# Optimization experiments

Measured on AMD Instinct MI355X. Metric: run time of the kernel, lower is better.

The kernel has to match this reference:

```python
import jax, jax.numpy as jnp
import numpy as np

N, C, H, W = 16, 128, 128, 128


def setup_inputs() -> dict:
    key = jax.random.key(0)
    ks = jax.random.split(key, 7)
    s = 0.02
    return {
        "x": jax.random.normal(ks[0], (N, C, H, W), dtype=jnp.float32),
        "w_key": jax.random.normal(ks[1], (C, C), dtype=jnp.float32) * s,
        "b_key": jax.random.normal(ks[2], (C,), dtype=jnp.float32) * s,
        "w_query": jax.random.normal(ks[3], (C, C), dtype=jnp.float32) * s,
        "b_query": jax.random.normal(ks[4], (C,), dtype=jnp.float32) * s,
        "w_value": jax.random.normal(ks[5], (C, C), dtype=jnp.float32) * s,
        "b_value": jax.random.normal(ks[6], (C,), dtype=jnp.float32) * s,
        "gamma": jnp.zeros((1,), dtype=jnp.float32),
    }


def _conv1x1(x, w, b):
    # 1x1 conv: (N,C,H,W) x (O,C) -> (N,O,H,W)
    return jnp.einsum('nchw,oc->nohw', x, w) + b[None, :, None, None]


def reference(x, w_key, b_key, w_query, b_query, w_value, b_value, gamma):
    k = _conv1x1(x, w_key, b_key)
    q = _conv1x1(x, w_query, b_query)
    v = _conv1x1(x, w_value, b_value)
    k_size = x.shape[1]  # output_channel
    scale = jnp.asarray(k_size, x.dtype) ** 0.5
    # similarity[n,o,w,v] = sum_h k[n,o,h,w] * q[n,o,h,v]  (k^T over H @ q)
    sim = jnp.einsum('nohw,nohv->nowv', k, q) / scale
    # softmax over dim=2 (the first W axis)
    attn = jax.nn.softmax(sim, axis=2)
    # out[n,o,h,v] = sum_w v[n,o,h,w] * attn[n,o,w,v]
    out = jnp.einsum('nohw,nowv->nohv', v, attn)
    return gamma[0] * out + x
```

## Files before the change

### kernel.cpp

```cpp
#include <hip/hip_runtime.h>
#include <hip/hip_bf16.h>
#include <math.h>

#define CN      128
#define HWN     16384
#define NBATCH  16
#define PLANE   (CN * HWN)
#define TSTRIDE ((size_t)NBATCH * PLANE)

typedef __attribute__((ext_vector_type(8))) short  short8;
typedef __attribute__((ext_vector_type(4))) float  float4v;

__device__ __forceinline__ unsigned short f2b(float f) {
    __hip_bfloat16 h = __float2bfloat16(f);
    return *reinterpret_cast<unsigned short*>(&h);
}
__device__ __forceinline__ unsigned packbf(float lo, float hi) {
    return (unsigned)f2b(lo) | ((unsigned)f2b(hi) << 16);
}
__device__ __forceinline__ float bf2f(unsigned short u) {
    union { unsigned i; float f; } x; x.i = ((unsigned)u) << 16; return x.f;
}

__global__ void prep_kernel(const float* __restrict__ wk, const float* __restrict__ bk,
                            const float* __restrict__ wq, const float* __restrict__ bq,
                            const float* __restrict__ wv, const float* __restrict__ bv,
                            unsigned short* __restrict__ wbf, float* __restrict__ bias)
{
    int i = blockIdx.x * 256 + threadIdx.x;
    int tensor = i >> 14, oc = i & 16383;
    const float* w = tensor == 0 ? wk : (tensor == 1 ? wq : wv);
    wbf[i] = f2b(w[oc]);
    if (i < 384) {
        const float* b = i < 128 ? bk : (i < 256 ? bq : bv);
        bias[i] = b[i & 127];
    }
}

__global__ __launch_bounds__(256) void kqv_kernel(
    const float* __restrict__ x, const unsigned short* __restrict__ wbf,
    const float* __restrict__ bias, unsigned short* __restrict__ kqv)
{
    __shared__ unsigned Xl[64 * 68];

    const int n   = blockIdx.y;
    const int hw0 = blockIdx.x * 64;
    const int t    = threadIdx.x;
    const int lane = t & 63, wv = t >> 6;
    const int l15  = lane & 15, quad = lane >> 4;

    const float* xp = x + (size_t)n * PLANE + hw0 + lane;
    #pragma unroll
    for (int it = 0; it < 4; ++it) {
        const int c0 = (wv * 4 + it) * 8;
        float v[8];
        #pragma unroll
        for (int j = 0; j < 8; ++j) v[j] = xp[(size_t)(c0 + j) * HWN];
        uint4 u;
        u.x = packbf(v[0], v[1]); u.y = packbf(v[2], v[3]);
        u.z = packbf(v[4], v[5]); u.w = packbf(v[6], v[7]);
        *(uint4*)&Xl[lane * 68 + c0 / 2] = u;
    }
    __syncthreads();

    short8 bfr[4][4];
    #pragma unroll
    for (int nt = 0; nt < 4; ++nt)
        #pragma unroll
        for (int k = 0; k < 4; ++k)
            bfr[nt][k] = *(const short8*)&Xl[(nt * 16 + l15) * 68 + quad * 4 + k * 16];

    for (int mt = 0; mt < 6; ++mt) {
        const int o0 = wv * 96 + mt * 16;
        short8 afr[4];
        #pragma unroll
        for (int k = 0; k < 4; ++k)
            afr[k] = *(const short8*)&wbf[(o0 + l15) * CN + quad * 8 + k * 32];
        float b0 = bias[o0 + quad * 4 + 0], b1 = bias[o0 + quad * 4 + 1];
        float b2 = bias[o0 + quad * 4 + 2], b3 = bias[o0 + quad * 4 + 3];

        #pragma unroll
        for (int nt = 0; nt < 4; ++nt) {
            float4v acc = {b0, b1, b2, b3};
            #pragma unroll
            for (int k = 0; k < 4; ++k)
                acc = __builtin_amdgcn_mfma_f32_16x16x32_bf16(afr[k], bfr[nt][k], acc, 0, 0, 0);
            #pragma unroll
            for (int r = 0; r < 4; ++r) {
                const int oo = o0 + quad * 4 + r;
                const size_t idx = (size_t)(oo >> 7) * TSTRIDE
                                 + ((size_t)n * CN + (oo & 127)) * HWN
                                 + hw0 + nt * 16 + l15;
                kqv[idx] = f2b(acc[r]);
            }
        }
    }
}

__global__ __launch_bounds__(256) void attn_kernel(
    const unsigned short* __restrict__ kqv, const float* __restrict__ x,
    const float* __restrict__ gamma, float* __restrict__ out)
{
    __shared__ unsigned lds[17408];
    unsigned* Kt = lds;
    unsigned* Qt = lds + 8704;
    unsigned short* At = (unsigned short*)lds;

    const int no = blockIdx.x;
    const unsigned short* Kg = kqv + (size_t)no * HWN;
    const unsigned short* Qg = Kg + TSTRIDE;
    const unsigned short* Vg = Kg + 2 * TSTRIDE;

    const int t = threadIdx.x, lane = t & 63, wv = t >> 6;
    const int l15 = lane & 15, quad = lane >> 4;

    #pragma unroll
    for (int p = 0; p < 8; ++p) {
        const int w  = (p & 1) * 64 + lane;
        const int h0 = ((p >> 1) * 4 + wv) * 8;
        unsigned short kv[8], qv[8];
        #pragma unroll
        for (int j = 0; j < 8; ++j) {
            kv[j] = Kg[(h0 + j) * 128 + w];
            qv[j] = Qg[(h0 + j) * 128 + w];
        }
        uint4 a, b;
        a.x = (unsigned)kv[0] | ((unsigned)kv[1] << 16); a.y = (unsigned)kv[2] | ((unsigned)kv[3] << 16);
        a.z = (unsigned)kv[4] | ((unsigned)kv[5] << 16); a.w = (unsigned)kv[6] | ((unsigned)kv[7] << 16);
        b.x = (unsigned)qv[0] | ((unsigned)qv[1] << 16); b.y = (unsigned)qv[2] | ((unsigned)qv[3] << 16);
        b.z = (unsigned)qv[4] | ((unsigned)qv[5] << 16); b.w = (unsigned)qv[6] | ((unsigned)qv[7] << 16);
        *(uint4*)&Kt[w * 68 + h0 / 2] = a;
        *(uint4*)&Qt[w * 68 + h0 / 2] = b;
    }
    __syncthreads();

    const int v0 = wv * 32;
    float4v acc1[2][8];
    #pragma unroll
    for (int mt = 0; mt < 2; ++mt)
        #pragma unroll
        for (int nt = 0; nt < 8; ++nt) acc1[mt][nt] = (float4v){0.f, 0.f, 0.f, 0.f};

    {
        short8 afr[2][4];
        #pragma unroll
        for (int mt = 0; mt < 2; ++mt)
            #pragma unroll
            for (int k = 0; k < 4; ++k)
                afr[mt][k] = *(const short8*)&Qt[(v0 + mt * 16 + l15) * 68 + quad * 4 + k * 16];
        #pragma unroll
        for (int nt = 0; nt < 8; ++nt) {
            short8 bfr[4];
            #pragma unroll
            for (int k = 0; k < 4; ++k)
                bfr[k] = *(const short8*)&Kt[(nt * 16 + l15) * 68 + quad * 4 + k * 16];
            #pragma unroll
            for (int mt = 0; mt < 2; ++mt)
                #pragma unroll
                for (int k = 0; k < 4; ++k)
                    acc1[mt][nt] = __builtin_amdgcn_mfma_f32_16x16x32_bf16(afr[mt][k], bfr[k], acc1[mt][nt], 0, 0, 0);
        }
    }
    __syncthreads();

    const float sc = 0.08838834764831845f;
    #pragma unroll
    for (int mt = 0; mt < 2; ++mt)
        #pragma unroll
        for (int r = 0; r < 4; ++r) {
            float m = -INFINITY;
            #pragma unroll
            for (int nt = 0; nt < 8; ++nt) {
                acc1[mt][nt][r] *= sc;
                m = fmaxf(m, acc1[mt][nt][r]);
            }
            #pragma unroll
            for (int d = 1; d < 16; d <<= 1) m = fmaxf(m, __shfl_xor(m, d, 64));
            float s = 0.f;
            #pragma unroll
            for (int nt = 0; nt < 8; ++nt) {
                const float e = __expf(acc1[mt][nt][r] - m);
                acc1[mt][nt][r] = e;
                s += e;
            }
            #pragma unroll
            for (int d = 1; d < 16; d <<= 1) s += __shfl_xor(s, d, 64);
            const float inv = 1.0f / s;
            const int v = v0 + mt * 16 + quad * 4 + r;
            #pragma unroll
            for (int nt = 0; nt < 8; ++nt)
                At[v * 136 + nt * 16 + l15] = f2b(acc1[mt][nt][r] * inv);
        }
    __syncthreads();

    const int h0 = wv * 32;
    float4v acc2[2][8];
    #pragma unroll
    for (int mt = 0; mt < 2; ++mt)
        #pragma unroll
        for (int nt = 0; nt < 8; ++nt) acc2[mt][nt] = (float4v){0.f, 0.f, 0.f, 0.f};

    {
        short8 vfr[2][4];
        #pragma unroll
        for (int mt = 0; mt < 2; ++mt)
            #pragma unroll
            for (int k = 0; k < 4; ++k)
                vfr[mt][k] = *(const short8*)&Vg[(h0 + mt * 16 + l15) * 128 + quad * 8 + k * 32];
        #pragma unroll
        for (int nt = 0; nt < 8; ++nt) {
            short8 bfr[4];
            #pragma unroll
            for (int k = 0; k < 4; ++k)
                bfr[k] = *(const short8*)&At[(nt * 16 + l15) * 136 + quad * 8 + k * 32];
            #pragma unroll
            for (int mt = 0; mt < 2; ++mt)
                #pragma unroll
                for (int k = 0; k < 4; ++k)
                    acc2[mt][nt] = __builtin_amdgcn_mfma_f32_16x16x32_bf16(vfr[mt][k], bfr[k], acc2[mt][nt], 0, 0, 0);
        }
    }

    const float g = gamma[0];
    const float* xp = x + (size_t)no * HWN;
    float*       op = out + (size_t)no * HWN;
    #pragma unroll
    for (int mt = 0; mt < 2; ++mt)
        #pragma unroll
        for (int nt = 0; nt < 8; ++nt)
            #pragma unroll
            for (int r = 0; r < 4; ++r) {
                const int h = h0 + mt * 16 + quad * 4 + r;
                const int v = nt * 16 + l15;
                const int idx = h * 128 + v;
                op[idx] = fmaf(g, acc2[mt][nt][r], xp[idx]);
            }
}

extern "C" void kernel_launch(void* const* d_in, const int* in_sizes, int n_in,
                              void* d_out, int out_size, void* d_ws, size_t ws_size,
                              hipStream_t stream) {
    const float* x     = (const float*)d_in[0];
    const float* wk    = (const float*)d_in[1];
    const float* bk    = (const float*)d_in[2];
    const float* wq    = (const float*)d_in[3];
    const float* bq    = (const float*)d_in[4];
    const float* wv    = (const float*)d_in[5];
    const float* bv    = (const float*)d_in[6];
    const float* gamma = (const float*)d_in[7];
    float* out = (float*)d_out;

    unsigned short* wbf  = (unsigned short*)d_ws;
    float*          bias = (float*)((char*)d_ws + (192 << 10));
    unsigned short* kqv  = (unsigned short*)((char*)d_ws + (256 << 10));

    prep_kernel<<<192, 256, 0, stream>>>(wk, bk, wq, bq, wv, bv, wbf, bias);
    dim3 gA(HWN / 64, NBATCH);
    kqv_kernel<<<gA, 256, 0, stream>>>(x, wbf, bias, kqv);
    attn_kernel<<<NBATCH * CN, 256, 0, stream>>>(kqv, x, gamma, out);
}
```

Measured before the change: 429.1 us.

## Store K and Q in pre-transposed h8-blocked layout so attention skips LDS staging

After: 476.6 us. +11.1%, slower.

```diff
diff --git a/kernel.cpp b/kernel.cpp
--- a/kernel.cpp
+++ b/kernel.cpp
@@ -17,9 +17,6 @@
 }
 __device__ __forceinline__ unsigned packbf(float lo, float hi) {
     return (unsigned)f2b(lo) | ((unsigned)f2b(hi) << 16);
-}
-__device__ __forceinline__ float bf2f(unsigned short u) {
-    union { unsigned i; float f; } x; x.i = ((unsigned)u) << 16; return x.f;
 }
 
 __global__ void prep_kernel(const float* __restrict__ wk, const float* __restrict__ bk,
@@ -41,57 +38,97 @@
     const float* __restrict__ x, const unsigned short* __restrict__ wbf,
     const float* __restrict__ bias, unsigned short* __restrict__ kqv)
 {
-    __shared__ unsigned Xl[64 * 68];
-
-    const int n   = blockIdx.y;
-    const int hw0 = blockIdx.x * 64;
-    const int t    = threadIdx.x;
-    const int lane = t & 63, wv = t >> 6;
-    const int l15  = lane & 15, quad = lane >> 4;
-
-    const float* xp = x + (size_t)n * PLANE + hw0 + lane;
-    #pragma unroll
-    for (int it = 0; it < 4; ++it) {
-        const int c0 = (wv * 4 + it) * 8;
-        float v[8];
-        #pragma unroll
-        for (int j = 0; j < 8; ++j) v[j] = xp[(size_t)(c0 + j) * HWN];
-        uint4 u;
-        u.x = packbf(v[0], v[1]); u.y = packbf(v[2], v[3]);
-        u.z = packbf(v[4], v[5]); u.w = packbf(v[6], v[7]);
-        *(uint4*)&Xl[lane * 68 + c0 / 2] = u;
-    }
-    __syncthreads();
-
-    short8 bfr[4][4];
-    #pragma unroll
-    for (int nt = 0; nt < 4; ++nt)
-        #pragma unroll
-        for (int k = 0; k < 4; ++k)
-            bfr[nt][k] = *(const short8*)&Xl[(nt * 16 + l15) * 68 + quad * 4 + k * 16];
-
-    for (int mt = 0; mt < 6; ++mt) {
-        const int o0 = wv * 96 + mt * 16;
-        short8 afr[4];
-        #pragma unroll
-        for (int k = 0; k < 4; ++k)
-            afr[k] = *(const short8*)&wbf[(o0 + l15) * CN + quad * 8 + k * 32];
-        float b0 = bias[o0 + quad * 4 + 0], b1 = bias[o0 + quad * 4 + 1];
-        float b2 = bias[o0 + quad * 4 + 2], b3 = bias[o0 + quad * 4 + 3];
-
-        #pragma unroll
-        for (int nt = 0; nt < 4; ++nt) {
-            float4v acc = {b0, b1, b2, b3};
-            #pragma unroll
-            for (int k = 0; k < 4; ++k)
-                acc = __builtin_amdgcn_mfma_f32_16x16x32_bf16(afr[k], bfr[nt][k], acc, 0, 0, 0);
-            #pragma unroll
-            for (int r = 0; r < 4; ++r) {
-                const int oo = o0 + quad * 4 + r;
-                const size_t idx = (size_t)(oo >> 7) * TSTRIDE
-                                 + ((size_t)n * CN + (oo & 127)) * HWN
-                                 + hw0 + nt * 16 + l15;
-                kqv[idx] = f2b(acc[r]);
+    __shared__ unsigned Xc[128 * 68];
+    __shared__ unsigned short Tk[4][16 * 136];
+
+    const int h8 = blockIdx.x >> 2, wq = blockIdx.x & 3, n = blockIdx.y;
+    const int h0 = h8 * 8;
+    const int t = threadIdx.x, lane = t & 63, wv = t >> 6;
+    const int l15 = lane & 15, quad = lane >> 4;
+    unsigned short* T = Tk[wv];
+
+    for (int chunk = 0; chunk < 2; ++chunk) {
+        const int w0 = wq * 32 + chunk * 16;
+        __syncthreads();
+
+        {
+            const int hwl = t & 127, half = t >> 7;
+            const int wl = hwl >> 3, dh = hwl & 7;
+            const float* xp = x + (size_t)n * PLANE + (size_t)(h0 + dh) * 128 + w0 + wl;
+            #pragma unroll
+            for (int i = 0; i < 8; ++i) {
+                const int c0 = (half * 8 + i) * 8;
+                float v[8];
+                #pragma unroll
+                for (int cc = 0; cc < 8; ++cc) v[cc] = xp[(size_t)(c0 + cc) * HWN];
+                uint4 u;
+                u.x = packbf(v[0], v[1]); u.y = packbf(v[2], v[3]);
+                u.z = packbf(v[4], v[5]); u.w = packbf(v[6], v[7]);
+                *(uint4*)&Xc[hwl * 68 + c0 / 2] = u;
+            }
+        }
+        __syncthreads();
+
+        short8 afr[8][4];
+        #pragma unroll
+        for (int mt = 0; mt < 8; ++mt)
+            #pragma unroll
+            for (int k = 0; k < 4; ++k)
+                afr[mt][k] = *(const short8*)&Xc[(mt * 16 + l15) * 68 + k * 16 + quad * 4];
+
+        for (int nt = 0; nt < 6; ++nt) {
+            const int ob = (nt * 4 + wv) * 16;
+            short8 bfr[4];
+            #pragma unroll
+            for (int k = 0; k < 4; ++k)
+                bfr[k] = *(const short8*)&wbf[(ob + l15) * CN + k * 32 + quad * 8];
+            const float bb = bias[ob + l15];
+            float4v acc[8];
+            #pragma unroll
+            for (int mt = 0; mt < 8; ++mt) acc[mt] = (float4v){bb, bb, bb, bb};
+            #pragma unroll
+            for (int mt = 0; mt < 8; ++mt)
+                #pragma unroll
+                for (int k = 0; k < 4; ++k)
+                    acc[mt] = __builtin_amdgcn_mfma_f32_16x16x32_bf16(afr[mt][k], bfr[k], acc[mt], 0, 0, 0);
+
+            #pragma unroll
+            for (int mt = 0; mt < 8; ++mt) {
+                uint2 p;
+                p.x = packbf(acc[mt][0], acc[mt][1]);
+                p.y = packbf(acc[mt][2], acc[mt][3]);
+                *(uint2*)&T[l15 * 136 + mt * 16 + quad * 4] = p;
+            }
+
+            const int tensor = ob >> 7;
+            const int oo = ob & 127;
+            if (tensor < 2) {
+                const int row = lane >> 2, s = lane & 3;
+                unsigned short* dst = kqv + (size_t)tensor * TSTRIDE
+                                    + ((size_t)n * CN + oo + row) * HWN + h8 * 1024;
+                #pragma unroll
+                for (int j = 0; j < 4; ++j) {
+                    uint4 u = *(const uint4*)&T[row * 136 + (s + 4 * j) * 8];
+                    *(uint4*)&dst[(w0 + s + 4 * j) * 8] = u;
+                }
+            } else {
+                const int o = lane >> 2, g = lane & 3;
+                const int wlh = g & 1, dh2 = g >> 1;
+                unsigned short* dst = kqv + 2 * TSTRIDE + ((size_t)n * CN + oo + o) * HWN;
+                #pragma unroll
+                for (int j = 0; j < 4; ++j) {
+                    const int dh = j * 2 + dh2;
+                    unsigned short tmp[8];
+                    #pragma unroll
+                    for (int i = 0; i < 8; ++i)
+                        tmp[i] = T[o * 136 + (wlh * 8 + i) * 8 + dh];
+                    uint4 u;
+                    u.x = (unsigned)tmp[0] | ((unsigned)tmp[1] << 16);
+                    u.y = (unsigned)tmp[2] | ((unsigned)tmp[3] << 16);
+                    u.z = (unsigned)tmp[4] | ((unsigned)tmp[5] << 16);
+                    u.w = (unsigned)tmp[6] | ((unsigned)tmp[7] << 16);
+                    *(uint4*)&dst[(size_t)(h0 + dh) * 128 + w0 + wlh * 8] = u;
+                }
             }
         }
     }
@@ -101,67 +138,42 @@
     const unsigned short* __restrict__ kqv, const float* __restrict__ x,
     const float* __restrict__ gamma, float* __restrict__ out)
 {
-    __shared__ unsigned lds[17408];
-    unsigned* Kt = lds;
-    unsigned* Qt = lds + 8704;
-    unsigned short* At = (unsigned short*)lds;
+    __shared__ unsigned short At[128 * 136];
 
     const int no = blockIdx.x;
-    const unsigned short* Kg = kqv + (size_t)no * HWN;
-    const unsigned short* Qg = Kg + TSTRIDE;
-    const unsigned short* Vg = Kg + 2 * TSTRIDE;
+    const unsigned short* KT = kqv + (size_t)no * HWN;
+    const unsigned short* QT = KT + TSTRIDE;
+    const unsigned short* Vg = KT + 2 * TSTRIDE;
 
     const int t = threadIdx.x, lane = t & 63, wv = t >> 6;
     const int l15 = lane & 15, quad = lane >> 4;
 
-    #pragma unroll
-    for (int p = 0; p < 8; ++p) {
-        const int w  = (p & 1) * 64 + lane;
-        const int h0 = ((p >> 1) * 4 + wv) * 8;
-        unsigned short kv[8], qv[8];
-        #pragma unroll
-        for (int j = 0; j < 8; ++j) {
-            kv[j] = Kg[(h0 + j) * 128 + w];
-            qv[j] = Qg[(h0 + j) * 128 + w];
-        }
-        uint4 a, b;
-        a.x = (unsigned)kv[0] | ((unsigned)kv[1] << 16); a.y = (unsigned)kv[2] | ((unsigned)kv[3] << 16);
-        a.z = (unsigned)kv[4] | ((unsigned)kv[5] << 16); a.w = (unsigned)kv[6] | ((unsigned)kv[7] << 16);
-        b.x = (unsigned)qv[0] | ((unsigned)qv[1] << 16); b.y = (unsigned)qv[2] | ((unsigned)qv[3] << 16);
-        b.z = (unsigned)qv[4] | ((unsigned)qv[5] << 16); b.w = (unsigned)qv[6] | ((unsigned)qv[7] << 16);
-        *(uint4*)&Kt[w * 68 + h0 / 2] = a;
-        *(uint4*)&Qt[w * 68 + h0 / 2] = b;
-    }
-    __syncthreads();
-
     const int v0 = wv * 32;
+    short8 afr[2][4];
+    #pragma unroll
+    for (int mt = 0; mt < 2; ++mt)
+        #pragma unroll
+        for (int k = 0; k < 4; ++k)
+            afr[mt][k] = *(const short8*)&QT[(k * 4 + quad) * 1024 + (v0 + mt * 16 + l15) * 8];
+
     float4v acc1[2][8];
     #pragma unroll
     for (int mt = 0; mt < 2; ++mt)
         #pragma unroll
         for (int nt = 0; nt < 8; ++nt) acc1[mt][nt] = (float4v){0.f, 0.f, 0.f, 0.f};
 
-    {
-        short8 afr[2][4];
+    #pragma unroll
+    for (int nt = 0; nt < 8; ++nt) {
+        short8 bfr[4];
+        #pragma unroll
+        for (int k = 0; k < 4; ++k)
+            bfr[k] = *(const short8*)&KT[(k * 4 + quad) * 1024 + (nt * 16 + l15) * 8];
         #pragma unroll
         for (int mt = 0; mt < 2; ++mt)
             #pragma unroll
             for (int k = 0; k < 4; ++k)
-                afr[mt][k] = *(const short8*)&Qt[(v0 + mt * 16 + l15) * 68 + quad * 4 + k * 16];
-        #pragma unroll
-        for (int nt = 0; nt < 8; ++nt) {
-            short8 bfr[4];
-            #pragma unroll
-            for (int k = 0; k < 4; ++k)
-                bfr[k] = *(const short8*)&Kt[(nt * 16 + l15) * 68 + quad * 4 + k * 16];
-            #pragma unroll
-            for (int mt = 0; mt < 2; ++mt)
-                #pragma unroll
-                for (int k = 0; k < 4; ++k)
-                    acc1[mt][nt] = __builtin_amdgcn_mfma_f32_16x16x32_bf16(afr[mt][k], bfr[k], acc1[mt][nt], 0, 0, 0);
-        }
-    }
-    __syncthreads();
+                acc1[mt][nt] = __builtin_amdgcn_mfma_f32_16x16x32_bf16(afr[mt][k], bfr[k], acc1[mt][nt], 0, 0, 0);
+    }
 
     const float sc = 0.08838834764831845f;
     #pragma unroll
@@ -194,31 +206,30 @@
     __syncthreads();
 
     const int h0 = wv * 32;
+    short8 vfr[2][4];
+    #pragma unroll
+    for (int mt = 0; mt < 2; ++mt)
+        #pragma unroll
+        for (int k = 0; k < 4; ++k)
+            vfr[mt][k] = *(const short8*)&Vg[(h0 + mt * 16 + l15) * 128 + k * 32 + quad * 8];
+
     float4v acc2[2][8];
     #pragma unroll
     for (int mt = 0; mt < 2; ++mt)
         #pragma unroll
         for (int nt = 0; nt < 8; ++nt) acc2[mt][nt] = (float4v){0.f, 0.f, 0.f, 0.f};
 
-    {
-        short8 vfr[2][4];
+    #pragma unroll
+    for (int nt = 0; nt < 8; ++nt) {
+        short8 bfr[4];
+        #pragma unroll
+        for (int k = 0; k < 4; ++k)
+            bfr[k] = *(const short8*)&At[(nt * 16 + l15) * 136 + k * 32 + quad * 8];
         #pragma unroll
         for (int mt = 0; mt < 2; ++mt)
             #pragma unroll
             for (int k = 0; k < 4; ++k)
-                vfr[mt][k] = *(const short8*)&Vg[(h0 + mt * 16 + l15) * 128 + quad * 8 + k * 32];
-        #pragma unroll
-        for (int nt = 0; nt < 8; ++nt) {
-            short8 bfr[4];
-            #pragma unroll
-            for (int k = 0; k < 4; ++k)
-                bfr[k] = *(const short8*)&At[(nt * 16 + l15) * 136 + quad * 8 + k * 32];
-            #pragma unroll
-            for (int mt = 0; mt < 2; ++mt)
-                #pragma unroll
-                for (int k = 0; k < 4; ++k)
-                    acc2[mt][nt] = __builtin_amdgcn_mfma_f32_16x16x32_bf16(vfr[mt][k], bfr[k], acc2[mt][nt], 0, 0, 0);
-        }
+                acc2[mt][nt] = __builtin_amdgcn_mfma_f32_16x16x32_bf16(vfr[mt][k], bfr[k], acc2[mt][nt], 0, 0, 0);
     }
 
     const float g = gamma[0];
@@ -230,9 +241,7 @@
         for (int nt = 0; nt < 8; ++nt)
             #pragma unroll
             for (int r = 0; r < 4; ++r) {
-                const int h = h0 + mt * 16 + quad * 4 + r;
-                const int v = nt * 16 + l15;
-                const int idx = h * 128 + v;
+                const int idx = (h0 + mt * 16 + quad * 4 + r) * 128 + nt * 16 + l15;
                 op[idx] = fmaf(g, acc2[mt][nt][r], xp[idx]);
             }
 }
@@ -255,7 +264,7 @@
     unsigned short* kqv  = (unsigned short*)((char*)d_ws + (256 << 10));
 
     prep_kernel<<<192, 256, 0, stream>>>(wk, bk, wq, bq, wv, bv, wbf, bias);
-    dim3 gA(HWN / 64, NBATCH);
+    dim3 gA(64, NBATCH);
     kqv_kernel<<<gA, 256, 0, stream>>>(x, wbf, bias, kqv);
     attn_kernel<<<NBATCH * CN, 256, 0, stream>>>(kqv, x, gamma, out);
 }
```
